# Performance work log

Measured on AMD Instinct MI355X. Metric: run time of the kernel, lower is better.

Reference implementation:

```python
import jax, jax.numpy as jnp
import numpy as np

B, L, E, D, A = 256, 196, 2048, 1024, 512


def setup_inputs() -> dict:
    key = jax.random.key(0)
    ks = jax.random.split(key, 9)
    enc_scale = 1.0 / np.sqrt(E)
    dec_scale = 1.0 / np.sqrt(D)
    att_scale = 1.0 / np.sqrt(A)
    return {
        "encoder_out": jax.random.normal(ks[0], (B, L, E), dtype=jnp.float32),
        "decoder_hidden": jax.random.normal(ks[1], (B, D), dtype=jnp.float32),
        "mask1": jax.random.randint(ks[2], (B, L), 0, 2, dtype=jnp.int32),
        "We": jax.random.uniform(ks[3], (E, A), jnp.float32, -enc_scale, enc_scale),
        "be": jax.random.uniform(ks[4], (A,), jnp.float32, -enc_scale, enc_scale),
        "Wd": jax.random.uniform(ks[5], (D, A), jnp.float32, -dec_scale, dec_scale),
        "bd": jax.random.uniform(ks[6], (A,), jnp.float32, -dec_scale, dec_scale),
        "wf": jax.random.uniform(ks[7], (A,), jnp.float32, -att_scale, att_scale),
        "bf": jax.random.uniform(ks[8], (), jnp.float32, -att_scale, att_scale),
    }


def reference(encoder_out, decoder_hidden, mask1, We, be, Wd, bd, wf, bf):
    # att1: [B, L, A]; att2: [B, A]
    att1 = jnp.einsum('ble,ea->bla', encoder_out, We) + be
    att2 = jnp.einsum('bd,da->ba', decoder_hidden, Wd) + bd
    # scores: [B, L]
    att = jnp.einsum('bla,a->bl', jnp.tanh(att1 + att2[:, None, :]), wf) + bf
    att = jnp.where(mask1 == 0, jnp.float32(-1e9), att)
    alpha = jax.nn.softmax(att, axis=1)
    # weighted sum over regions: [B, E]
    awe = jnp.einsum('ble,bl->be', encoder_out, alpha)
    return (awe, alpha)
```

## Files before the change

### kernel.cpp

```cpp
#include <hip/hip_runtime.h>
#include <hip/hip_bf16.h>


#define B_ 256
#define L_ 196
#define E_ 2048
#define D_ 1024
#define A_ 512
#define M_TOT (B_ * L_)

typedef __attribute__((ext_vector_type(8))) short bf16x8;
typedef __attribute__((ext_vector_type(4))) float f32x4;

static __device__ __forceinline__ unsigned short f2bf(float f) {
    union { float f; unsigned u; } u{f};
    unsigned r = u.u + 0x7fffu + ((u.u >> 16) & 1u);
    return (unsigned short)(r >> 16);
}
static __device__ __forceinline__ unsigned int pk2(float x, float y) {
    __hip_bfloat162 h = __float22bfloat162_rn(float2{x, y});
    return *reinterpret_cast<unsigned int*>(&h);
}
static __device__ __forceinline__ void gload_lds16(const void* g, void* l) {
    __builtin_amdgcn_global_load_lds(
        (const __attribute__((address_space(1))) unsigned int*)g,
        (__attribute__((address_space(3))) unsigned int*)l, 16, 0, 0);
}

__global__ __launch_bounds__(256) void k_wepack(const float* __restrict__ We,
                                                unsigned short* __restrict__ WeP) {
    int i = blockIdx.x * 256 + threadIdx.x;
    int k = i >> 9, n = i & 511;
    int kb = k >> 5, slot = (k >> 3) & 3, e = k & 7;
    int slotE = slot ^ ((n >> 1) & 3);
    WeP[(kb << 14) + (n << 5) + (slotE << 3) + e] = f2bf(We[i]);
}

__global__ __launch_bounds__(256) void k_bias2(const float* __restrict__ dec,
                                               const float* __restrict__ Wd,
                                               const float* __restrict__ be,
                                               const float* __restrict__ bd,
                                               float* __restrict__ bias2) {
    int b = blockIdx.x, t = threadIdx.x;
    __shared__ float ds[D_];
    for (int i = t; i < D_; i += 256) ds[i] = dec[b * D_ + i];
    __syncthreads();
    for (int a0 = 0; a0 < A_; a0 += 256) {
        int a = a0 + t;
        float acc = 0.f;
        #pragma unroll 8
        for (int d = 0; d < D_; d++) acc += ds[d] * Wd[d * A_ + a];
        bias2[b * A_ + a] = acc + be[a] + bd[a];
    }
}

__global__ __launch_bounds__(256, 3) void k_gemm_score(
        const float* __restrict__ enc,
        const unsigned short* __restrict__ WeP,
        const float* __restrict__ bias2,
        const float* __restrict__ wf,
        float* __restrict__ scoresP) {
    __shared__ __align__(16) unsigned short aL[3][4096];
    __shared__ __align__(16) unsigned short bL[3][4096];
    __shared__ float score_lds[4][64];

    const int tid = threadIdx.x;
    const int raw = blockIdx.x;
    const int wg = (raw & 7) * 196 + (raw >> 3);
    const int mt = wg >> 2, nt = wg & 3;
    const int m0 = mt * 128;

    const int lane = tid & 63, wid = tid >> 6;
    const int wm = wid >> 1, wn = wid & 1;
    const int kg = lane >> 4, lr = lane & 15;

    const int ar = tid >> 1, kh = tid & 1;
    const float* aSrc = enc + (size_t)(m0 + ar) * E_ + kh * 16;
    const int sw = (ar >> 1) & 3;
    const int aOff0 = ar * 32 + ((((kh << 1) | 0) ^ sw) << 3);
    const int aOff1 = ar * 32 + ((((kh << 1) | 1) ^ sw) << 3);

    const unsigned short* bSrc = WeP + nt * 4096 + tid * 8;

    auto stageB = [&](int kb, int buf) {
        const unsigned short* s = bSrc + (kb << 14);
        gload_lds16(s,        &bL[buf][tid * 8]);
        gload_lds16(s + 2048, &bL[buf][2048 + tid * 8]);
    };
    auto loadA = [&](float4 (&v)[4], int kb) {
        const float* p = aSrc + (kb << 5);
        v[0] = *reinterpret_cast<const float4*>(p);
        v[1] = *reinterpret_cast<const float4*>(p + 4);
        v[2] = *reinterpret_cast<const float4*>(p + 8);
        v[3] = *reinterpret_cast<const float4*>(p + 12);
    };
    auto writeA = [&](const float4 (&v)[4], int buf) {
        uint4 q0, q1;
        q0.x = pk2(v[0].x, v[0].y); q0.y = pk2(v[0].z, v[0].w);
        q0.z = pk2(v[1].x, v[1].y); q0.w = pk2(v[1].z, v[1].w);
        q1.x = pk2(v[2].x, v[2].y); q1.y = pk2(v[2].z, v[2].w);
        q1.z = pk2(v[3].x, v[3].y); q1.w = pk2(v[3].z, v[3].w);
        *reinterpret_cast<uint4*>(&aL[buf][aOff0]) = q0;
        *reinterpret_cast<uint4*>(&aL[buf][aOff1]) = q1;
    };

    f32x4 acc[4][4];
    #pragma unroll
    for (int i = 0; i < 4; i++)
        #pragma unroll
        for (int j = 0; j < 4; j++) acc[i][j] = (f32x4){0.f, 0.f, 0.f, 0.f};

    auto computeTile = [&](int buf) {
        bf16x8 bfr[4];
        #pragma unroll
        for (int j = 0; j < 4; j++) {
            int n = wn * 64 + j * 16 + lr;
            bfr[j] = *reinterpret_cast<const bf16x8*>(
                &bL[buf][n * 32 + ((kg ^ ((n >> 1) & 3)) << 3)]);
        }
        #pragma unroll
        for (int i = 0; i < 4; i++) {
            int row = wm * 64 + i * 16 + lr;
            bf16x8 af = *reinterpret_cast<const bf16x8*>(
                &aL[buf][row * 32 + ((kg ^ ((row >> 1) & 3)) << 3)]);
            #pragma unroll
            for (int j = 0; j < 4; j++)
                acc[i][j] = __builtin_amdgcn_mfma_f32_16x16x32_bf16(
                    af, bfr[j], acc[i][j], 0, 0, 0);
        }
    };

    float4 avA[4], avB[4], avC[4];
    int t = 0;

    auto step = [&](float4 (&wr)[4], float4 (&ld)[4],
                    int sbuf, int cbuf, int wbuf) {
        stageB(t + 2, sbuf);
        __builtin_amdgcn_sched_barrier(0);
        loadA(ld, t + 3);
        __builtin_amdgcn_sched_barrier(0);
        computeTile(cbuf);
        writeA(wr, wbuf);
        asm volatile("s_waitcnt vmcnt(6) lgkmcnt(0)" ::: "memory");
        __builtin_amdgcn_s_barrier();
        __builtin_amdgcn_sched_barrier(0);
        t++;
    };

    stageB(0, 0);
    stageB(1, 1);
    __builtin_amdgcn_sched_barrier(0);
    loadA(avA, 0);
    loadA(avB, 1);
    loadA(avC, 2);
    __builtin_amdgcn_sched_barrier(0);
    writeA(avA, 0);
    asm volatile("s_waitcnt vmcnt(8) lgkmcnt(0)" ::: "memory");
    __builtin_amdgcn_s_barrier();
    __builtin_amdgcn_sched_barrier(0);

    for (int u = 0; u < 20; u++) {
        step(avB, avA, 2, 0, 1);
        step(avC, avB, 0, 1, 2);
        step(avA, avC, 1, 2, 0);
    }
    step(avB, avA, 2, 0, 1);
    stageB(63, 0);
    __builtin_amdgcn_sched_barrier(0);
    computeTile(1);
    writeA(avC, 2);
    asm volatile("s_waitcnt vmcnt(6) lgkmcnt(0)" ::: "memory");
    __builtin_amdgcn_s_barrier();
    __builtin_amdgcn_sched_barrier(0);
    computeTile(2);
    writeA(avA, 0);
    asm volatile("s_waitcnt vmcnt(0) lgkmcnt(0)" ::: "memory");
    __builtin_amdgcn_s_barrier();
    __builtin_amdgcn_sched_barrier(0);
    computeTile(0);

    #pragma unroll
    for (int i = 0; i < 4; i++) {
        #pragma unroll
        for (int r = 0; r < 4; r++) {
            int Rw = i * 16 + kg * 4 + r;
            int gm = m0 + wm * 64 + Rw;
            int bg = gm / L_;
            float sum = 0.f;
            #pragma unroll
            for (int j = 0; j < 4; j++) {
                int C = nt * 128 + wn * 64 + j * 16 + lr;
                float x = acc[i][j][r] + bias2[bg * A_ + C];
                float ex = __expf(2.f * x);
                sum += wf[C] * (1.f - 2.f * __builtin_amdgcn_rcpf(ex + 1.f));
            }
            #pragma unroll
            for (int mk = 1; mk < 16; mk <<= 1) sum += __shfl_xor(sum, mk);
            if (lr == 0) score_lds[wid][Rw] = sum;
        }
    }
    __syncthreads();
    if (tid < 128) {
        int wmp = tid >> 6, rl = tid & 63;
        float s = score_lds[wmp * 2][rl] + score_lds[wmp * 2 + 1][rl];
        scoresP[nt * M_TOT + m0 + wmp * 64 + rl] = s;
    }
}

__global__ __launch_bounds__(256) void k_softmax(const float* __restrict__ scoresP,
                                                 const int* __restrict__ mask,
                                                 const float* __restrict__ bfp,
                                                 float* __restrict__ alpha) {
    int b = blockIdx.x, t = threadIdx.x;
    float bfv = bfp[0];
    float v = -INFINITY;
    if (t < L_) {
        int idx = b * L_ + t;
        float sc = scoresP[idx] + scoresP[M_TOT + idx] +
                   scoresP[2 * M_TOT + idx] + scoresP[3 * M_TOT + idx];
        v = (mask[idx] == 0) ? -1e9f : (sc + bfv);
    }
    __shared__ float redm[4], reds[4];
    float m = v;
    #pragma unroll
    for (int s = 1; s < 64; s <<= 1) m = fmaxf(m, __shfl_xor(m, s));
    int w = t >> 6;
    if ((t & 63) == 0) redm[w] = m;
    __syncthreads();
    m = fmaxf(fmaxf(redm[0], redm[1]), fmaxf(redm[2], redm[3]));
    float e = (t < L_) ? expf(v - m) : 0.f;
    float s = e;
    #pragma unroll
    for (int k = 1; k < 64; k <<= 1) s += __shfl_xor(s, k);
    if ((t & 63) == 0) reds[w] = s;
    __syncthreads();
    s = reds[0] + reds[1] + reds[2] + reds[3];
    if (t < L_) alpha[b * L_ + t] = e / s;
}

__global__ __launch_bounds__(256) void k_awe(const float* __restrict__ enc,
                                             const float* __restrict__ alpha,
                                             float* __restrict__ awe) {
    int b = blockIdx.y, ec = blockIdx.x, t = threadIdx.x;
    int g = t >> 6, lt = t & 63;
    __shared__ float al[L_];
    __shared__ float4 red[256];
    if (t < L_) al[t] = alpha[b * L_ + t];
    __syncthreads();
    int e0 = (ec << 8) + (lt << 2);
    const float* base = enc + (size_t)b * L_ * E_ + e0;
    float4 acc = {0.f, 0.f, 0.f, 0.f};
    int l0 = g * 49;
    #pragma unroll 7
    for (int l = l0; l < l0 + 49; l++) {
        float4 v = *reinterpret_cast<const float4*>(base + (size_t)l * E_);
        float a = al[l];
        acc.x += a * v.x; acc.y += a * v.y; acc.z += a * v.z; acc.w += a * v.w;
    }
    red[t] = acc;
    __syncthreads();
    if (t < 64) {
        float4 r0 = red[t], r1 = red[64 + t], r2 = red[128 + t], r3 = red[192 + t];
        float4 o;
        o.x = r0.x + r1.x + r2.x + r3.x;
        o.y = r0.y + r1.y + r2.y + r3.y;
        o.z = r0.z + r1.z + r2.z + r3.z;
        o.w = r0.w + r1.w + r2.w + r3.w;
        *reinterpret_cast<float4*>(awe + b * E_ + (ec << 8) + (t << 2)) = o;
    }
}

extern "C" void kernel_launch(void* const* d_in, const int* in_sizes, int n_in,
                              void* d_out, int out_size, void* d_ws, size_t ws_size,
                              hipStream_t stream) {
    const float* enc  = (const float*)d_in[0];
    const float* dec  = (const float*)d_in[1];
    const int*   mask = (const int*)d_in[2];
    const float* We   = (const float*)d_in[3];
    const float* be   = (const float*)d_in[4];
    const float* Wd   = (const float*)d_in[5];
    const float* bd   = (const float*)d_in[6];
    const float* wf   = (const float*)d_in[7];
    const float* bf   = (const float*)d_in[8];

    float* awe   = (float*)d_out;
    float* alpha = awe + (size_t)B_ * E_;

    char* ws = (char*)d_ws;
    unsigned short* WeP = (unsigned short*)ws;
    float* bias2   = (float*)(ws + 2097152);
    float* scoresP = (float*)(ws + 2621440);

    hipLaunchKernelGGL(k_wepack, dim3((E_ * A_) / 256), dim3(256), 0, stream, We, WeP);
    hipLaunchKernelGGL(k_bias2, dim3(B_), dim3(256), 0, stream, dec, Wd, be, bd, bias2);
    hipLaunchKernelGGL(k_gemm_score, dim3(1568), dim3(256), 0, stream,
                       enc, WeP, bias2, wf, scoresP);
    hipLaunchKernelGGL(k_softmax, dim3(B_), dim3(256), 0, stream, scoresP, mask, bf, alpha);
    hipLaunchKernelGGL(k_awe, dim3(8, B_), dim3(256), 0, stream, enc, alpha, awe);
}
```

Measured before the change: 437.6 us.

## Stage fp32 encoder tiles via async LDS loads and batch bias GEMV rows

The score GEMM no longer loads encoder rows into registers, converts them to bf16 and writes them to LDS. It now copies fp32 tiles straight into a swizzled LDS buffer with global_load_lds and converts to bf16 while building the MFMA operands. This removes the register round-trip and the hand-scheduled triple-buffer pipeline, replacing it with a simple double buffer and a __syncthreads each step. In exchange the kernel uses much more LDS per block, so fewer blocks fit per CU, and it leaves less prefetch slack. Separately, the decoder bias GEMV now handles four batch rows per block, so each Wd element is read once for four rows, at the cost of launching fewer blocks.

```diff
diff --git a/kernel.cpp b/kernel.cpp
--- a/kernel.cpp
+++ b/kernel.cpp
@@ -41,16 +41,25 @@
                                                const float* __restrict__ be,
                                                const float* __restrict__ bd,
                                                float* __restrict__ bias2) {
-    int b = blockIdx.x, t = threadIdx.x;
-    __shared__ float ds[D_];
-    for (int i = t; i < D_; i += 256) ds[i] = dec[b * D_ + i];
-    __syncthreads();
-    for (int a0 = 0; a0 < A_; a0 += 256) {
-        int a = a0 + t;
-        float acc = 0.f;
-        #pragma unroll 8
-        for (int d = 0; d < D_; d++) acc += ds[d] * Wd[d * A_ + a];
-        bias2[b * A_ + a] = acc + be[a] + bd[a];
+    int b0 = blockIdx.x * 4, t = threadIdx.x;
+    __shared__ float ds[4][D_];
+    for (int i = t; i < 4 * D_; i += 256) ds[i >> 10][i & 1023] = dec[(size_t)b0 * D_ + i];
+    __syncthreads();
+    #pragma unroll
+    for (int p = 0; p < 2; p++) {
+        int a = p * 256 + t;
+        float a0 = 0.f, a1 = 0.f, a2 = 0.f, a3 = 0.f;
+        #pragma unroll 4
+        for (int d = 0; d < D_; d++) {
+            float w = Wd[d * A_ + a];
+            a0 += ds[0][d] * w; a1 += ds[1][d] * w;
+            a2 += ds[2][d] * w; a3 += ds[3][d] * w;
+        }
+        float bb = be[a] + bd[a];
+        bias2[(b0 + 0) * A_ + a] = a0 + bb;
+        bias2[(b0 + 1) * A_ + a] = a1 + bb;
+        bias2[(b0 + 2) * A_ + a] = a2 + bb;
+        bias2[(b0 + 3) * A_ + a] = a3 + bb;
     }
 }
 
@@ -60,8 +69,8 @@
         const float* __restrict__ bias2,
         const float* __restrict__ wf,
         float* __restrict__ scoresP) {
-    __shared__ __align__(16) unsigned short aL[3][4096];
-    __shared__ __align__(16) unsigned short bL[3][4096];
+    __shared__ __align__(16) float aF[2][4096];
+    __shared__ __align__(16) unsigned short bL[2][4096];
     __shared__ float score_lds[4][64];
 
     const int tid = threadIdx.x;
@@ -74,34 +83,18 @@
     const int wm = wid >> 1, wn = wid & 1;
     const int kg = lane >> 4, lr = lane & 15;
 
-    const int ar = tid >> 1, kh = tid & 1;
-    const float* aSrc = enc + (size_t)(m0 + ar) * E_ + kh * 16;
-    const int sw = (ar >> 1) & 3;
-    const int aOff0 = ar * 32 + ((((kh << 1) | 0) ^ sw) << 3);
-    const int aOff1 = ar * 32 + ((((kh << 1) | 1) ^ sw) << 3);
-
+    const int sA = (lane & 7) ^ (lane >> 3);
+    const float* aSrc0 = enc + (size_t)(m0 + (tid >> 3)) * E_ + sA * 4;
     const unsigned short* bSrc = WeP + nt * 4096 + tid * 8;
 
-    auto stageB = [&](int kb, int buf) {
-        const unsigned short* s = bSrc + (kb << 14);
-        gload_lds16(s,        &bL[buf][tid * 8]);
-        gload_lds16(s + 2048, &bL[buf][2048 + tid * 8]);
-    };
-    auto loadA = [&](float4 (&v)[4], int kb) {
-        const float* p = aSrc + (kb << 5);
-        v[0] = *reinterpret_cast<const float4*>(p);
-        v[1] = *reinterpret_cast<const float4*>(p + 4);
-        v[2] = *reinterpret_cast<const float4*>(p + 8);
-        v[3] = *reinterpret_cast<const float4*>(p + 12);
-    };
-    auto writeA = [&](const float4 (&v)[4], int buf) {
-        uint4 q0, q1;
-        q0.x = pk2(v[0].x, v[0].y); q0.y = pk2(v[0].z, v[0].w);
-        q0.z = pk2(v[1].x, v[1].y); q0.w = pk2(v[1].z, v[1].w);
-        q1.x = pk2(v[2].x, v[2].y); q1.y = pk2(v[2].z, v[2].w);
-        q1.z = pk2(v[3].x, v[3].y); q1.w = pk2(v[3].z, v[3].w);
-        *reinterpret_cast<uint4*>(&aL[buf][aOff0]) = q0;
-        *reinterpret_cast<uint4*>(&aL[buf][aOff1]) = q1;
+    auto stage = [&](int kb, int buf) {
+        #pragma unroll
+        for (int c = 0; c < 4; c++)
+            gload_lds16(aSrc0 + (size_t)c * 32 * E_ + (kb << 5),
+                        &aF[buf][(c * 256 + tid) * 4]);
+        const unsigned short* sb = bSrc + (kb << 14);
+        gload_lds16(sb,        &bL[buf][tid * 8]);
+        gload_lds16(sb + 2048, &bL[buf][2048 + tid * 8]);
     };
 
     f32x4 acc[4][4];
@@ -121,63 +114,31 @@
         #pragma unroll
         for (int i = 0; i < 4; i++) {
             int row = wm * 64 + i * 16 + lr;
-            bf16x8 af = *reinterpret_cast<const bf16x8*>(
-                &aL[buf][row * 32 + ((kg ^ ((row >> 1) & 3)) << 3)]);
+            int r7 = row & 7;
+            const float* base = &aF[buf][row * 32];
+            float4 f0 = *reinterpret_cast<const float4*>(
+                base + ((((kg << 1) | 0) ^ r7) << 2));
+            float4 f1 = *reinterpret_cast<const float4*>(
+                base + ((((kg << 1) | 1) ^ r7) << 2));
+            union { uint4 q; bf16x8 v; } u;
+            u.q.x = pk2(f0.x, f0.y); u.q.y = pk2(f0.z, f0.w);
+            u.q.z = pk2(f1.x, f1.y); u.q.w = pk2(f1.z, f1.w);
             #pragma unroll
             for (int j = 0; j < 4; j++)
                 acc[i][j] = __builtin_amdgcn_mfma_f32_16x16x32_bf16(
-                    af, bfr[j], acc[i][j], 0, 0, 0);
+                    u.v, bfr[j], acc[i][j], 0, 0, 0);
         }
     };
 
-    float4 avA[4], avB[4], avC[4];
-    int t = 0;
-
-    auto step = [&](float4 (&wr)[4], float4 (&ld)[4],
-                    int sbuf, int cbuf, int wbuf) {
-        stageB(t + 2, sbuf);
-        __builtin_amdgcn_sched_barrier(0);
-        loadA(ld, t + 3);
-        __builtin_amdgcn_sched_barrier(0);
-        computeTile(cbuf);
-        writeA(wr, wbuf);
-        asm volatile("s_waitcnt vmcnt(6) lgkmcnt(0)" ::: "memory");
-        __builtin_amdgcn_s_barrier();
-        __builtin_amdgcn_sched_barrier(0);
-        t++;
-    };
-
-    stageB(0, 0);
-    stageB(1, 1);
-    __builtin_amdgcn_sched_barrier(0);
-    loadA(avA, 0);
-    loadA(avB, 1);
-    loadA(avC, 2);
-    __builtin_amdgcn_sched_barrier(0);
-    writeA(avA, 0);
-    asm volatile("s_waitcnt vmcnt(8) lgkmcnt(0)" ::: "memory");
-    __builtin_amdgcn_s_barrier();
-    __builtin_amdgcn_sched_barrier(0);
-
-    for (int u = 0; u < 20; u++) {
-        step(avB, avA, 2, 0, 1);
-        step(avC, avB, 0, 1, 2);
-        step(avA, avC, 1, 2, 0);
-    }
-    step(avB, avA, 2, 0, 1);
-    stageB(63, 0);
-    __builtin_amdgcn_sched_barrier(0);
-    computeTile(1);
-    writeA(avC, 2);
-    asm volatile("s_waitcnt vmcnt(6) lgkmcnt(0)" ::: "memory");
-    __builtin_amdgcn_s_barrier();
-    __builtin_amdgcn_sched_barrier(0);
-    computeTile(2);
-    writeA(avA, 0);
-    asm volatile("s_waitcnt vmcnt(0) lgkmcnt(0)" ::: "memory");
-    __builtin_amdgcn_s_barrier();
-    __builtin_amdgcn_sched_barrier(0);
-    computeTile(0);
+    stage(0, 0);
+    __syncthreads();
+    int buf = 0;
+    for (int kb = 0; kb < 64; kb++) {
+        if (kb < 63) stage(kb + 1, buf ^ 1);
+        computeTile(buf);
+        __syncthreads();
+        buf ^= 1;
+    }
 
     #pragma unroll
     for (int i = 0; i < 4; i++) {
@@ -292,7 +253,7 @@
     float* scoresP = (float*)(ws + 2621440);
 
     hipLaunchKernelGGL(k_wepack, dim3((E_ * A_) / 256), dim3(256), 0, stream, We, WeP);
-    hipLaunchKernelGGL(k_bias2, dim3(B_), dim3(256), 0, stream, dec, Wd, be, bd, bias2);
+    hipLaunchKernelGGL(k_bias2, dim3(B_ / 4), dim3(256), 0, stream, dec, Wd, be, bd, bias2);
     hipLaunchKernelGGL(k_gemm_score, dim3(1568), dim3(256), 0, stream,
                        enc, WeP, bias2, wf, scoresP);
     hipLaunchKernelGGL(k_softmax, dim3(B_), dim3(256), 0, stream, scoresP, mask, bf, alpha);
```

Result: slower. 588.9 us (+34.6%).
